# Performance work log

Measured on AMD Instinct MI355X. Metric: run time of the kernel, lower is better.

The kernel has to match this reference:

```python
import jax, jax.numpy as jnp
import numpy as np

ATTR_LEN = [2, 4, 4, 2, 6]
CUM = np.concatenate(([0], np.cumsum(ATTR_LEN)))  # [0,2,6,10,12,18]
B, S, D, V = 4096, 200, 64, 100000


def setup_inputs() -> dict:
    key = jax.random.key(0)
    ks = jax.random.split(key, 10)
    x = jax.random.randint(ks[0], (B, S), 0, V)
    # one-hot labels per attribute, concatenated -> [B, 18]
    y_parts = []
    for i, al in enumerate(ATTR_LEN):
        lab = jax.random.randint(jax.random.fold_in(ks[1], i), (B,), 0, al)
        y_parts.append(jax.nn.one_hot(lab, al, dtype=jnp.float32))
    y = jnp.concatenate(y_parts, axis=1)
    emb_table = jax.random.normal(ks[2], (V, D), jnp.float32) * 0.02
    emb_table = emb_table.at[0].set(0.0)  # padding_idx=0
    att_w = jax.random.normal(ks[3], (5, D), jnp.float32) * 0.1
    att_b = jax.random.normal(ks[4], (5,), jnp.float32) * 0.1
    W0 = jax.random.normal(ks[5], (ATTR_LEN[0], D), jnp.float32) * 0.1
    W1 = jax.random.normal(ks[6], (ATTR_LEN[1], D), jnp.float32) * 0.1
    W2 = jax.random.normal(ks[7], (ATTR_LEN[2], D), jnp.float32) * 0.1
    W3 = jax.random.normal(ks[8], (ATTR_LEN[3], D), jnp.float32) * 0.1
    W4 = jax.random.normal(ks[9], (ATTR_LEN[4], D), jnp.float32) * 0.1
    return {"x": x, "y": y, "emb_table": emb_table, "att_w": att_w,
            "att_b": att_b, "W0": W0, "W1": W1, "W2": W2, "W3": W3, "W4": W4}


def reference(x, y, emb_table, att_w, att_b, W0, W1, W2, W3, W4):
    embed = emb_table[x]  # [B, S, D] gather (padding row is zero)
    # 5 per-attribute additive tanh-attention heads, batched over k.
    # Softmax over seq axis is independent per head, so stacking is exact.
    att_u = jnp.tanh(jnp.einsum('bsd,kd->bsk', embed, att_w) + att_b)  # [B,S,5]
    score = jax.nn.softmax(att_u, axis=1)                              # [B,S,5]
    user_rep = jnp.einsum('bsd,bsk->bkd', embed, score)                # [B,5,D]
    Ws = [W0, W1, W2, W3, W4]
    # per-task bias-free linear heads, concatenated -> [B, 18]
    W_user = jnp.concatenate([user_rep[:, i] @ Ws[i].T for i in range(5)], axis=1)
    logits = []
    loss = jnp.float32(0.0)
    for i in range(5):
        Wc = W_user[:, CUM[i]:CUM[i + 1]]
        yc = y[:, CUM[i]:CUM[i + 1]]
        # partial_training=False -> ob = ones -> all rows kept;
        # obj = exp(sum(W*y)) / sum_j exp(W_j)  ==  softmax picked at label
        logp = jax.nn.log_softmax(Wc, axis=1)
        loss = loss + (-jnp.sum(logp * yc) / Wc.shape[0])
        logits.append(jax.nn.softmax(Wc, axis=1))
    logit = jnp.concatenate(logits, axis=1)  # [B, 18]
    return logit, loss
```

## Files before the change

### kernel.cpp

```cpp
#include <hip/hip_runtime.h>
#include <math.h>

#define Bsz 4096
#define Ssz 200
#define Dsz 64
#define NK  5
#define NT  512
#define ROWH 72

typedef _Float16 half_t;
typedef _Float16 h2 __attribute__((ext_vector_type(2)));

__device__ inline h2 shfl_xor_h2(h2 v, int m) {
    int iv = __builtin_bit_cast(int, v);
    iv = __shfl_xor(iv, m);
    return __builtin_bit_cast(h2, iv);
}

__device__ inline h2 pk(float a, float b) {
    return __builtin_bit_cast(h2, __builtin_amdgcn_cvt_pkrtz(a, b));
}

__device__ inline float fdot2(h2 a, h2 b, float c) {
#if __has_builtin(__builtin_amdgcn_fdot2)
    return __builtin_amdgcn_fdot2(a, b, c, false);
#else
    return c + (float)a.x * (float)b.x + (float)a.y * (float)b.y;
#endif
}

__device__ inline float fast_tanh(float x) {
    float e = __expf(-2.0f * fabsf(x));
    float r = (1.0f - e) / (1.0f + e);
    return copysignf(r, x);
}

__global__ void zero_loss_kernel(float* loss) {
    if (threadIdx.x == 0) *loss = 0.0f;
}

__global__ __launch_bounds__(NT, 8) void tan_kernel(
    const int* __restrict__ x, const float* __restrict__ y,
    const float* __restrict__ emb_table,
    const float* __restrict__ att_w, const float* __restrict__ att_b,
    const float* __restrict__ W0, const float* __restrict__ W1,
    const float* __restrict__ W2, const float* __restrict__ W3,
    const float* __restrict__ W4,
    float* __restrict__ out_logit, float* __restrict__ loss_out)
{
    __shared__ alignas(16) half_t embh[Ssz * ROWH];
    __shared__ alignas(16) float  att[NK][Ssz];
    __shared__ alignas(16) h2     awh[NK * 32];
    __shared__ alignas(16) half_t urph[8][NK][Dsz];
    __shared__ alignas(16) int    xs[Ssz];
    __shared__ float wu[18];

    const int b   = blockIdx.x;
    const int tid = threadIdx.x;
    const int w   = tid >> 6;
    const int l   = tid & 63;

    if (tid < Ssz) xs[tid] = x[b * Ssz + tid];
    if (tid >= 256 && tid < 256 + NK * 32) {
        const int t = tid - 256;
        awh[t] = (h2){(half_t)att_w[2 * t], (half_t)att_w[2 * t + 1]};
    }
    __syncthreads();

    {
        float4 v[7];
#pragma unroll
        for (int p = 0; p < 7; ++p) {
            int i = tid + NT * p;
            if (i > Ssz * 16 - 1) i = Ssz * 16 - 1;
            const int s = i >> 4, c = i & 15;
            v[p] = ((const float4*)(emb_table + (size_t)xs[s] * Dsz))[c];
        }
#pragma unroll
        for (int p = 0; p < 7; ++p) {
            const int i = tid + NT * p;
            if (p < 6 || i < Ssz * 16) {
                const int s = i >> 4, c = i & 15;
                h2 lo = pk(v[p].x, v[p].y);
                h2 hi = pk(v[p].z, v[p].w);
                uint2 u = { __builtin_bit_cast(unsigned, lo),
                            __builtin_bit_cast(unsigned, hi) };
                *(uint2*)(embh + s * ROWH + c * 4) = u;
            }
        }
    }
    __syncthreads();

    if (tid < 2 * Ssz) {
        const int s = tid >> 1, h = tid & 1;
        union { uint4 q[4]; h2 hh[16]; } ue;
        const uint4* rp = (const uint4*)(embh + s * ROWH + h * 32);
#pragma unroll
        for (int i = 0; i < 4; ++i) ue.q[i] = rp[i];
        float acc[NK];
#pragma unroll 1
        for (int k = 0; k < NK; ++k) {
            union { uint4 q[4]; h2 hh[16]; } ua;
            const uint4* ap = (const uint4*)(awh + k * 32 + h * 16);
#pragma unroll
            for (int i = 0; i < 4; ++i) ua.q[i] = ap[i];
            float a = 0.f;
#pragma unroll
            for (int i = 0; i < 16; ++i) a = fdot2(ue.hh[i], ua.hh[i], a);
            acc[k] = a;
        }
#pragma unroll
        for (int k = 0; k < NK; ++k) acc[k] += __shfl_xor(acc[k], 1);
        if (h == 0) {
#pragma unroll
            for (int k = 0; k < NK; ++k) att[k][s] = fast_tanh(acc[k] + att_b[k]);
        }
    }
    __syncthreads();

    if (w < NK) {
        const int k = w;
        float vals[4];
        float mx = -1e30f;
#pragma unroll
        for (int j = 0; j < 4; ++j) {
            int s = l + 64 * j;
            vals[j] = (s < Ssz) ? att[k][s] : -1e30f;
            mx = fmaxf(mx, vals[j]);
        }
#pragma unroll
        for (int m = 32; m >= 1; m >>= 1) mx = fmaxf(mx, __shfl_xor(mx, m));
        float sum = 0.f;
#pragma unroll
        for (int j = 0; j < 4; ++j) {
            vals[j] = __expf(vals[j] - mx);
            sum += vals[j];
        }
#pragma unroll
        for (int m = 32; m >= 1; m >>= 1) sum += __shfl_xor(sum, m);
        float inv = 1.0f / sum;
#pragma unroll
        for (int j = 0; j < 4; ++j) {
            int s = l + 64 * j;
            if (s < Ssz) att[k][s] = vals[j] * inv;
        }
    }
    __syncthreads();

    {
        const int c = tid & 7;
        const int j = tid >> 3;
        h2 acc[NK][4];
#pragma unroll
        for (int k = 0; k < NK; ++k)
#pragma unroll
            for (int i = 0; i < 4; ++i) acc[k][i] = (h2){(half_t)0, (half_t)0};
#pragma unroll
        for (int t = 0; t < 4; ++t) {
            const int s = j + 64 * t;
            if (s < Ssz) {
                union { uint4 q; h2 hh[4]; } u;
                u.q = *(const uint4*)(embh + s * ROWH + c * 8);
#pragma unroll
                for (int k = 0; k < NK; ++k) {
                    half_t f = (half_t)att[k][s];
                    h2 sc = (h2){f, f};
#pragma unroll
                    for (int i = 0; i < 4; ++i) acc[k][i] += u.hh[i] * sc;
                }
            }
        }
#pragma unroll
        for (int k = 0; k < NK; ++k)
#pragma unroll
            for (int i = 0; i < 4; ++i) {
                acc[k][i] += shfl_xor_h2(acc[k][i], 8);
                acc[k][i] += shfl_xor_h2(acc[k][i], 16);
                acc[k][i] += shfl_xor_h2(acc[k][i], 32);
            }
        if (l < 8) {
#pragma unroll
            for (int k = 0; k < NK; ++k) {
                union { h2 a[4]; uint4 q; } uu;
#pragma unroll
                for (int i = 0; i < 4; ++i) uu.a[i] = acc[k][i];
                *(uint4*)(&urph[w][k][l * 8]) = uu.q;
            }
        }
    }
    __syncthreads();

    for (int j = w; j < 18; j += 8) {
        const float* Wp; int g, c0;
        if      (j < 2)  { g = 0; c0 = 0;  Wp = W0; }
        else if (j < 6)  { g = 1; c0 = 2;  Wp = W1; }
        else if (j < 10) { g = 2; c0 = 6;  Wp = W2; }
        else if (j < 12) { g = 3; c0 = 10; Wp = W3; }
        else             { g = 4; c0 = 12; Wp = W4; }
        float urv = 0.f;
#pragma unroll
        for (int jj = 0; jj < 8; ++jj) urv += (float)urph[jj][g][l];
        float p = urv * Wp[(j - c0) * Dsz + l];
#pragma unroll
        for (int m = 32; m >= 1; m >>= 1) p += __shfl_xor(p, m);
        if (l == 0) wu[j] = p;
    }
    __syncthreads();

    if (w == 0) {
        float lossb = 0.f;
        if (l < NK) {
            const int LEN[5] = {2, 4, 4, 2, 6};
            const int C0[5]  = {0, 2, 6, 10, 12};
            const int g = l, c0 = C0[g], len = LEN[g];
            float* op = out_logit + (size_t)b * 18;
            const float* yp = y + (size_t)b * 18;
            float mx = -1e30f;
            for (int j = 0; j < len; ++j) mx = fmaxf(mx, wu[c0 + j]);
            float sum = 0.f;
            for (int j = 0; j < len; ++j) sum += __expf(wu[c0 + j] - mx);
            float inv = 1.0f / sum;
            float lse = mx + __logf(sum);
            for (int j = 0; j < len; ++j) {
                op[c0 + j] = __expf(wu[c0 + j] - mx) * inv;
                lossb += (lse - wu[c0 + j]) * yp[c0 + j];
            }
        }
#pragma unroll
        for (int m = 1; m <= 4; m <<= 1) lossb += __shfl_xor(lossb, m);
        if (l == 0) atomicAdd(loss_out, lossb * (1.0f / Bsz));
    }
}

extern "C" void kernel_launch(void* const* d_in, const int* in_sizes, int n_in,
                              void* d_out, int out_size, void* d_ws, size_t ws_size,
                              hipStream_t stream) {
    const int*   x   = (const int*)d_in[0];
    const float* y   = (const float*)d_in[1];
    const float* emb = (const float*)d_in[2];
    const float* aw  = (const float*)d_in[3];
    const float* ab  = (const float*)d_in[4];
    const float* W0  = (const float*)d_in[5];
    const float* W1  = (const float*)d_in[6];
    const float* W2  = (const float*)d_in[7];
    const float* W3  = (const float*)d_in[8];
    const float* W4  = (const float*)d_in[9];
    float* out  = (float*)d_out;
    float* loss = out + (size_t)Bsz * 18;

    zero_loss_kernel<<<1, 64, 0, stream>>>(loss);
    tan_kernel<<<Bsz, NT, 0, stream>>>(x, y, emb, aw, ab,
                                       W0, W1, W2, W3, W4, out, loss);
}
```

Measured before the change: 154.8 us.

## Overlay attention and partial-sum LDS buffers and pack scores as half2

```diff
diff --git a/kernel.cpp b/kernel.cpp
--- a/kernel.cpp
+++ b/kernel.cpp
@@ -7,6 +7,7 @@
 #define NK  5
 #define NT  512
 #define ROWH 72
+#define SPS 104
 
 typedef _Float16 half_t;
 typedef _Float16 h2 __attribute__((ext_vector_type(2)));
@@ -49,11 +50,14 @@
     float* __restrict__ out_logit, float* __restrict__ loss_out)
 {
     __shared__ alignas(16) half_t embh[Ssz * ROWH];
-    __shared__ alignas(16) float  att[NK][Ssz];
+    __shared__ alignas(16) char   ovl[8 * NK * Dsz * 2];
+    __shared__ alignas(16) h2     att_h2[NK * SPS];
     __shared__ alignas(16) h2     awh[NK * 32];
-    __shared__ alignas(16) half_t urph[8][NK][Dsz];
     __shared__ alignas(16) int    xs[Ssz];
     __shared__ float wu[18];
+
+    float*  att  = (float*)ovl;
+    half_t (*urph)[NK][Dsz] = (half_t(*)[NK][Dsz])ovl;
 
     const int b   = blockIdx.x;
     const int tid = threadIdx.x;
@@ -113,7 +117,8 @@
         for (int k = 0; k < NK; ++k) acc[k] += __shfl_xor(acc[k], 1);
         if (h == 0) {
 #pragma unroll
-            for (int k = 0; k < NK; ++k) att[k][s] = fast_tanh(acc[k] + att_b[k]);
+            for (int k = 0; k < NK; ++k)
+                att[k * Ssz + s] = fast_tanh(acc[k] + att_b[k]);
         }
     }
     __syncthreads();
@@ -125,7 +130,7 @@
 #pragma unroll
         for (int j = 0; j < 4; ++j) {
             int s = l + 64 * j;
-            vals[j] = (s < Ssz) ? att[k][s] : -1e30f;
+            vals[j] = (s < Ssz) ? att[k * Ssz + s] : -1e30f;
             mx = fmaxf(mx, vals[j]);
         }
 #pragma unroll
@@ -141,50 +146,57 @@
         float inv = 1.0f / sum;
 #pragma unroll
         for (int j = 0; j < 4; ++j) {
-            int s = l + 64 * j;
-            if (s < Ssz) att[k][s] = vals[j] * inv;
+            const int s = l + 64 * j;
+            float scv = vals[j] * inv;
+            float pnr = __shfl_xor(scv, 1);
+            if (s < Ssz && (l & 1) == 0)
+                att_h2[k * SPS + (s >> 1)] = pk(scv, pnr);
         }
     }
     __syncthreads();
 
     {
-        const int c = tid & 7;
-        const int j = tid >> 3;
-        h2 acc[NK][4];
+        const int c = tid & 15;
+        const int j = tid >> 4;
+        h2 acc[NK][2];
+#pragma unroll
+        for (int k = 0; k < NK; ++k) {
+            acc[k][0] = (h2){(half_t)0, (half_t)0};
+            acc[k][1] = (h2){(half_t)0, (half_t)0};
+        }
+#pragma unroll
+        for (int t = 0; t < 4; ++t) {
+            const int p = j + 32 * t;
+            if (p < 100) {
+                const int s0 = 2 * p;
+                union { uint2 q; h2 hh[2]; } e0, e1;
+                e0.q = *(const uint2*)(embh + s0 * ROWH + c * 4);
+                e1.q = *(const uint2*)(embh + (s0 + 1) * ROWH + c * 4);
+#pragma unroll
+                for (int k = 0; k < NK; ++k) {
+                    h2 sp = att_h2[k * SPS + p];
+                    h2 sc0 = (h2){sp.x, sp.x};
+                    h2 sc1 = (h2){sp.y, sp.y};
+                    acc[k][0] += e0.hh[0] * sc0;
+                    acc[k][1] += e0.hh[1] * sc0;
+                    acc[k][0] += e1.hh[0] * sc1;
+                    acc[k][1] += e1.hh[1] * sc1;
+                }
+            }
+        }
 #pragma unroll
         for (int k = 0; k < NK; ++k)
 #pragma unroll
-            for (int i = 0; i < 4; ++i) acc[k][i] = (h2){(half_t)0, (half_t)0};
-#pragma unroll
-        for (int t = 0; t < 4; ++t) {
-            const int s = j + 64 * t;
-            if (s < Ssz) {
-                union { uint4 q; h2 hh[4]; } u;
-                u.q = *(const uint4*)(embh + s * ROWH + c * 8);
-#pragma unroll
-                for (int k = 0; k < NK; ++k) {
-                    half_t f = (half_t)att[k][s];
-                    h2 sc = (h2){f, f};
-#pragma unroll
-                    for (int i = 0; i < 4; ++i) acc[k][i] += u.hh[i] * sc;
-                }
-            }
-        }
-#pragma unroll
-        for (int k = 0; k < NK; ++k)
-#pragma unroll
-            for (int i = 0; i < 4; ++i) {
-                acc[k][i] += shfl_xor_h2(acc[k][i], 8);
+            for (int i = 0; i < 2; ++i) {
                 acc[k][i] += shfl_xor_h2(acc[k][i], 16);
                 acc[k][i] += shfl_xor_h2(acc[k][i], 32);
             }
-        if (l < 8) {
+        if (l < 16) {
 #pragma unroll
             for (int k = 0; k < NK; ++k) {
-                union { h2 a[4]; uint4 q; } uu;
-#pragma unroll
-                for (int i = 0; i < 4; ++i) uu.a[i] = acc[k][i];
-                *(uint4*)(&urph[w][k][l * 8]) = uu.q;
+                union { h2 a[2]; uint2 q; } uu;
+                uu.a[0] = acc[k][0]; uu.a[1] = acc[k][1];
+                *(uint2*)(&urph[w][k][l * 4]) = uu.q;
             }
         }
     }
```

New measurement: 153.7 us. About the same (-0.7%).
